# Kernel optimization log

Hardware: AMD Instinct MI355X
Metric: run time of the kernel (lower is better)

Reference implementation:

```python
import jax, jax.numpy as jnp
import numpy as np

DIM = 2048
NUM_HEADS = 16
HEAD_DIM = DIM // NUM_HEADS  # 128
ROPE_BASE = 10000.0


def setup_inputs() -> dict:
    key = jax.random.key(0)
    k1, k2, k3 = jax.random.split(key, 3)
    B, S = 2, 2048
    x = jax.random.normal(k1, (B, S, DIM), dtype=jnp.float32)
    # causal mask: 1 where allowed (k <= q), 0 elsewhere
    mask = jnp.tril(jnp.ones((S, S), dtype=jnp.int32))
    # torch Linear(dim, 3*dim, bias=False): store transposed so y = x @ w
    w_qkv = jax.random.normal(k2, (DIM, 3 * DIM), dtype=jnp.float32) / np.sqrt(DIM)
    w_out = jax.random.normal(k3, (DIM, DIM), dtype=jnp.float32) / np.sqrt(DIM)
    return {"x": x, "w_qkv": w_qkv, "w_out": w_out, "mask": mask}


def _rope_cos_sin(seq_len, dtype):
    inv_freq = 1.0 / (ROPE_BASE ** (jnp.arange(0, HEAD_DIM, 2, dtype=jnp.float32) / HEAD_DIM))
    t = jnp.arange(seq_len, dtype=jnp.float32)
    freqs = t[:, None] * inv_freq[None, :]          # [S, D/2]
    emb = jnp.concatenate([freqs, freqs], axis=-1)  # [S, D]
    return jnp.cos(emb).astype(dtype), jnp.sin(emb).astype(dtype)


def _rotate_half(x):
    x1, x2 = jnp.split(x, 2, axis=-1)
    return jnp.concatenate([-x2, x1], axis=-1)


def reference(x, w_qkv, w_out, mask):
    B, S, _ = x.shape
    H, D = NUM_HEADS, HEAD_DIM
    qkv = x @ w_qkv                                   # [B, S, 3*dim]
    qkv = qkv.reshape(B, S, 3, H, D).transpose(2, 0, 3, 1, 4)  # [3, B, H, S, D]
    q, k, v = qkv[0], qkv[1], qkv[2]
    cos, sin = _rope_cos_sin(S, x.dtype)              # [S, D] broadcast over B,H
    q = q * cos + _rotate_half(q) * sin
    k = k * cos + _rotate_half(k) * sin
    scale = D ** -0.5
    score = jnp.einsum("bhqd,bhkd->bhqk", q, k) * scale
    score = jnp.where(mask == 0, -jnp.inf, score)
    attn = jax.nn.softmax(score, axis=-1)             # dropout = identity (eval)
    out = jnp.einsum("bhqk,bhkd->bhqd", attn, v)
    out = out.transpose(0, 2, 1, 3).reshape(B, S, H * D)
    return out @ w_out
```

## Files before the change

kernel.cpp:

```cpp
#include <hip/hip_runtime.h>

typedef __attribute__((ext_vector_type(8))) __bf16 bf16x8;
typedef __attribute__((ext_vector_type(4))) float f32x4;

__device__ __forceinline__ unsigned short f2bf(float x) {
  union { float f; unsigned int u; } v; v.f = x;
  unsigned int r = v.u + 0x7fffu + ((v.u >> 16) & 1u);
  return (unsigned short)(r >> 16);
}
__device__ __forceinline__ float bf2f(unsigned short x) {
  union { unsigned int u; float f; } v; v.u = ((unsigned int)x) << 16;
  return v.f;
}
__device__ __forceinline__ void g2l16(const void* g, void* l) {
  __builtin_amdgcn_global_load_lds((const __attribute__((address_space(1))) void*)g,
                                   (__attribute__((address_space(3))) void*)l, 16, 0, 0);
}

__global__ __launch_bounds__(256) void cvt_f32_bf16_k(const float* __restrict__ in,
                                                      unsigned short* __restrict__ out) {
  int i = blockIdx.x * 256 + threadIdx.x;
  float4 v = ((const float4*)in)[i];
  ushort4 o;
  o.x = f2bf(v.x); o.y = f2bf(v.y); o.z = f2bf(v.z); o.w = f2bf(v.w);
  ((ushort4*)out)[i] = o;
}

__global__ __launch_bounds__(256) void tr_cvt_k(const float* __restrict__ in,
                                                unsigned short* __restrict__ out,
                                                int R, int C) {
  __shared__ unsigned short t[64][65];
  int c0 = blockIdx.x * 64, r0 = blockIdx.y * 64;
  int tx = threadIdx.x & 63, tg = threadIdx.x >> 6;
#pragma unroll
  for (int i = 0; i < 16; i++) {
    int r = i * 4 + tg;
    t[r][tx] = f2bf(in[(size_t)(r0 + r) * C + c0 + tx]);
  }
  __syncthreads();
#pragma unroll
  for (int i = 0; i < 16; i++) {
    int c = i * 4 + tg;
    out[(size_t)(c0 + c) * R + r0 + tx] = t[tx][c];
  }
}

__global__ __launch_bounds__(256) void tr_b16_k(const unsigned short* __restrict__ in,
                                                unsigned short* __restrict__ out,
                                                int R, int C) {
  __shared__ unsigned short t[64][65];
  const size_t zoff = (size_t)blockIdx.z * R * C;
  int c0 = blockIdx.x * 64, r0 = blockIdx.y * 64;
  int tx = threadIdx.x & 63, tg = threadIdx.x >> 6;
#pragma unroll
  for (int i = 0; i < 16; i++) {
    int r = i * 4 + tg;
    t[r][tx] = in[zoff + (size_t)(r0 + r) * C + c0 + tx];
  }
  __syncthreads();
#pragma unroll
  for (int i = 0; i < 16; i++) {
    int c = i * 4 + tg;
    out[zoff + (size_t)(c0 + c) * R + r0 + tx] = t[tx][c];
  }
}

template <int EPI>
__global__ __launch_bounds__(256) void gemm_bt_k(const unsigned short* __restrict__ A,
                                                 const unsigned short* __restrict__ BT,
                                                 int K, int N,
                                                 float* __restrict__ outF,
                                                 unsigned short* __restrict__ oq,
                                                 unsigned short* __restrict__ ok,
                                                 unsigned short* __restrict__ ov) {
  __shared__ __align__(16) unsigned short lA[128 * 32];
  __shared__ __align__(16) unsigned short lB[128 * 32];
  const int tid = threadIdx.x;
  const int w = tid >> 6, lane = tid & 63;
  const int quad = lane >> 4, l16 = lane & 15;
  const int m0 = blockIdx.y * 128, n0 = blockIdx.x * 128;
  const int wm = (w >> 1) * 64, wn = (w & 1) * 64;
  f32x4 acc[4][4] = {};
  const unsigned short* gA = A + (size_t)(m0 + w * 16 + (lane >> 2)) * K + (lane & 3) * 8;
  const unsigned short* gB = BT + (size_t)(n0 + w * 16 + (lane >> 2)) * K + (lane & 3) * 8;
  char* lAw = (char*)lA + w * 1024 + lane * 16;
  char* lBw = (char*)lB + w * 1024 + lane * 16;
  const size_t rowskip = (size_t)64 * K;
  for (int k0 = 0; k0 < K; k0 += 32) {
    g2l16(gA + k0, lAw);
    g2l16(gA + k0 + rowskip, lAw + 4096);
    g2l16(gB + k0, lBw);
    g2l16(gB + k0 + rowskip, lBw + 4096);
    __syncthreads();
    bf16x8 af[4], bfv[4];
#pragma unroll
    for (int i = 0; i < 4; i++)
      af[i] = *(const bf16x8*)((const char*)lA + (wm + i * 16 + l16) * 64 + quad * 16);
#pragma unroll
    for (int j = 0; j < 4; j++)
      bfv[j] = *(const bf16x8*)((const char*)lB + (wn + j * 16 + l16) * 64 + quad * 16);
#pragma unroll
    for (int i = 0; i < 4; i++)
#pragma unroll
      for (int j = 0; j < 4; j++)
        acc[i][j] = __builtin_amdgcn_mfma_f32_16x16x32_bf16(af[i], bfv[j], acc[i][j], 0, 0, 0);
    __syncthreads();
  }
  if (EPI == 0) {
    const int which = n0 >> 11;
    const int h = (n0 >> 7) & 15;
    unsigned short* dst = (which == 0) ? oq : (which == 1) ? ok : ov;
#pragma unroll
    for (int i = 0; i < 4; i++) {
#pragma unroll
      for (int r = 0; r < 4; r++) {
        int mm = m0 + wm + i * 16 + quad * 4 + r;
        int b = mm >> 11, s = mm & 2047;
        size_t rb = ((size_t)(b * 16 + h) * 2048 + s) * 128;
#pragma unroll
        for (int j = 0; j < 4; j++)
          dst[rb + wn + j * 16 + l16] = f2bf(acc[i][j][r]);
      }
    }
  } else {
#pragma unroll
    for (int i = 0; i < 4; i++)
#pragma unroll
      for (int r = 0; r < 4; r++) {
        size_t rowb = (size_t)(m0 + wm + i * 16 + quad * 4 + r) * N;
#pragma unroll
        for (int j = 0; j < 4; j++)
          outF[rowb + n0 + wn + j * 16 + l16] = acc[i][j][r];
      }
  }
}

__global__ __launch_bounds__(256) void rope_k(unsigned short* __restrict__ buf, float scale) {
  int i = blockIdx.x * 256 + threadIdx.x;
  int d = i & 63;
  int s = (i >> 6) & 2047;
  int bh = i >> 17;
  size_t base = ((size_t)bh * 2048 + s) * 128;
  float a = bf2f(buf[base + d]);
  float b = bf2f(buf[base + 64 + d]);
  double theta = (double)s * exp2(-(double)d * (13.287712379549449 / 64.0));
  double sn, cs;
  sincos(theta, &sn, &cs);
  float c = (float)cs, sf = (float)sn;
  buf[base + d] = f2bf((a * c - b * sf) * scale);
  buf[base + 64 + d] = f2bf((b * c + a * sf) * scale);
}

__global__ __launch_bounds__(256, 2) void attn_k(const unsigned short* __restrict__ qb,
                                                 const unsigned short* __restrict__ kb,
                                                 const unsigned short* __restrict__ vt,
                                                 unsigned short* __restrict__ ob) {
  __shared__ __align__(16) unsigned short lK[64 * 128];
  __shared__ __align__(16) unsigned short lV[128 * 64];
  __shared__ __align__(16) __bf16 pbuf[4][32 * 72];
  const int tid = threadIdx.x;
  const int w = tid >> 6, lane = tid & 63;
  const int quad = lane >> 4, l16 = lane & 15;
  const int qt = (blockIdx.y < 16) ? (int)blockIdx.x : 15 - (int)blockIdx.x;
  const int bh = blockIdx.y;
  const int bi = bh >> 4, h = bh & 15;
  const int q0w = qt * 128 + w * 32;
  const unsigned short* qp = qb + (size_t)bh * 2048 * 128;
  const unsigned short* kp = kb + (size_t)bh * 2048 * 128;
  const unsigned short* vp = vt + (size_t)bh * 128 * 2048;
  __bf16* pw = pbuf[w];

  bf16x8 qf[2][4];
#pragma unroll
  for (int rg = 0; rg < 2; rg++) {
    const unsigned short* qr = qp + (size_t)(q0w + rg * 16 + l16) * 128 + quad * 8;
#pragma unroll
    for (int st = 0; st < 4; st++) qf[rg][st] = *(const bf16x8*)(qr + st * 32);
  }
  f32x4 o[2][8] = {};
  f32x4 lsum[2] = {};

  const int krow = tid >> 4;
  const int kcg = (tid & 15) ^ krow;
  const int vd = tid >> 3;
  const int vsg = (tid & 7) ^ ((tid >> 3) & 7);
  unsigned short* lKdst = lK + (size_t)tid * 8;
  unsigned short* lVdst = lV + (size_t)tid * 8;

  const int nkt = 2 * qt + 2;
  const int myNkt = (q0w + 31) / 64 + 1;
  for (int kt = 0; kt < nkt; kt++) {
    const int kt0 = kt * 64;
#pragma unroll
    for (int j = 0; j < 4; j++) {
      g2l16(kp + (size_t)(kt0 + j * 16 + krow) * 128 + kcg * 8, lKdst + j * 2048);
      g2l16(vp + (size_t)(j * 32 + vd) * 2048 + kt0 + vsg * 8, lVdst + j * 2048);
    }
    __syncthreads();
    if (kt < myNkt) {
      f32x4 sc[2][4] = {};
#pragma unroll
      for (int ct = 0; ct < 4; ct++) {
        const int nrow = ct * 16 + l16;
#pragma unroll
        for (int st = 0; st < 4; st++) {
          bf16x8 kf = *(const bf16x8*)(lK + ((size_t)nrow * 16 + ((st * 4 + quad) ^ l16)) * 8);
          sc[0][ct] = __builtin_amdgcn_mfma_f32_16x16x32_bf16(qf[0][st], kf, sc[0][ct], 0, 0, 0);
          sc[1][ct] = __builtin_amdgcn_mfma_f32_16x16x32_bf16(qf[1][st], kf, sc[1][ct], 0, 0, 0);
        }
      }
      const bool needmask = (kt == myNkt - 1);
#pragma unroll
      for (int rg = 0; rg < 2; rg++)
#pragma unroll
        for (int ct = 0; ct < 4; ct++) {
          const int col = kt0 + ct * 16 + l16;
          const int rowb = q0w + rg * 16 + quad * 4;
#pragma unroll
          for (int r = 0; r < 4; r++) {
            float s = sc[rg][ct][r];
            if (needmask && col > rowb + r) s = -1e30f;
            float e = __expf(s);
            lsum[rg][r] += e;
            pw[(rg * 16 + quad * 4 + r) * 72 + ct * 16 + l16] = (__bf16)e;
          }
        }
      bf16x8 pf[2][2];
#pragma unroll
      for (int rg = 0; rg < 2; rg++)
#pragma unroll
        for (int sb = 0; sb < 2; sb++)
          pf[rg][sb] = *(const bf16x8*)(pw + (rg * 16 + l16) * 72 + sb * 32 + quad * 8);
#pragma unroll
      for (int dt = 0; dt < 8; dt++) {
#pragma unroll
        for (int sb = 0; sb < 2; sb++) {
          bf16x8 vf = *(const bf16x8*)(lV +
              ((size_t)(dt * 16 + l16) * 8 + ((sb * 4 + quad) ^ (l16 & 7))) * 8);
          o[0][dt] = __builtin_amdgcn_mfma_f32_16x16x32_bf16(pf[0][sb], vf, o[0][dt], 0, 0, 0);
          o[1][dt] = __builtin_amdgcn_mfma_f32_16x16x32_bf16(pf[1][sb], vf, o[1][dt], 0, 0, 0);
        }
      }
    }
    __syncthreads();
  }
#pragma unroll
  for (int m = 1; m < 16; m <<= 1)
#pragma unroll
    for (int rg = 0; rg < 2; rg++)
#pragma unroll
      for (int r = 0; r < 4; r++)
        lsum[rg][r] += __shfl_xor(lsum[rg][r], m, 64);
  float inv[2][4];
#pragma unroll
  for (int rg = 0; rg < 2; rg++)
#pragma unroll
    for (int r = 0; r < 4; r++) inv[rg][r] = 1.0f / lsum[rg][r];
#pragma unroll
  for (int rg = 0; rg < 2; rg++)
#pragma unroll
    for (int dt = 0; dt < 8; dt++)
#pragma unroll
      for (int r = 0; r < 4; r++)
        ob[(size_t)(bi * 2048 + q0w + rg * 16 + quad * 4 + r) * 2048 + h * 128 + dt * 16 + l16] =
            f2bf(o[rg][dt][r] * inv[rg][r]);
}

extern "C" void kernel_launch(void* const* d_in, const int* in_sizes, int n_in,
                              void* d_out, int out_size, void* d_ws, size_t ws_size,
                              hipStream_t stream) {
  const float* x = (const float*)d_in[0];
  const float* wqkv = (const float*)d_in[1];
  const float* wout = (const float*)d_in[2];
  char* ws = (char*)d_ws;
  const size_t MiB = 1ull << 20;
  unsigned short* xb    = (unsigned short*)(ws + 0);
  unsigned short* wqkvT = (unsigned short*)(ws + 16 * MiB);
  unsigned short* woutT = (unsigned short*)(ws + 40 * MiB);
  unsigned short* qb    = (unsigned short*)(ws + 48 * MiB);
  unsigned short* kb    = (unsigned short*)(ws + 64 * MiB);
  unsigned short* vb    = (unsigned short*)(ws + 80 * MiB);
  unsigned short* vtb   = (unsigned short*)(ws + 96 * MiB);
  unsigned short* attnb = (unsigned short*)(ws + 112 * MiB);
  float* outF = (float*)d_out;

  cvt_f32_bf16_k<<<8192, 256, 0, stream>>>(x, xb);
  tr_cvt_k<<<dim3(96, 32), 256, 0, stream>>>(wqkv, wqkvT, 2048, 6144);
  tr_cvt_k<<<dim3(32, 32), 256, 0, stream>>>(wout, woutT, 2048, 2048);
  gemm_bt_k<0><<<dim3(48, 32), 256, 0, stream>>>(xb, wqkvT, 2048, 6144, nullptr, qb, kb, vb);
  rope_k<<<16384, 256, 0, stream>>>(qb, 0.08838834764831845f);
  rope_k<<<16384, 256, 0, stream>>>(kb, 1.0f);
  tr_b16_k<<<dim3(2, 32, 32), 256, 0, stream>>>(vb, vtb, 2048, 128);
  attn_k<<<dim3(16, 32), 256, 0, stream>>>(qb, kb, vtb, attnb);
  gemm_bt_k<1><<<dim3(16, 32), 256, 0, stream>>>(attnb, woutT, 2048, 2048, outF,
                                                 nullptr, nullptr, nullptr);
}
```

Before: 447.0 us.

## Widen GEMM K-tile with XOR-swizzled LDS, merge RoPE launches, use fast float trig

The GEMM now stages 64-wide K slices per iteration with an XOR swizzle on LDS chunk placement, which halves the barriers per K and is meant to avoid LDS bank conflicts on fragment reads. The two RoPE launches are merged into one grid that picks q or k from the block index. RoPE angle computation moves from double-precision exp2/sincos to float exp2f and __sincosf. The fast intrinsic loses accuracy for large angles (positions up to 2047), which may hurt numerical agreement with the reference.

```diff
diff --git a/kernel.cpp b/kernel.cpp
--- a/kernel.cpp
+++ b/kernel.cpp
@@ -73,37 +73,45 @@
                                                  unsigned short* __restrict__ oq,
                                                  unsigned short* __restrict__ ok,
                                                  unsigned short* __restrict__ ov) {
-  __shared__ __align__(16) unsigned short lA[128 * 32];
-  __shared__ __align__(16) unsigned short lB[128 * 32];
+  __shared__ __align__(16) unsigned short lA[128 * 64];
+  __shared__ __align__(16) unsigned short lB[128 * 64];
   const int tid = threadIdx.x;
   const int w = tid >> 6, lane = tid & 63;
   const int quad = lane >> 4, l16 = lane & 15;
   const int m0 = blockIdx.y * 128, n0 = blockIdx.x * 128;
   const int wm = (w >> 1) * 64, wn = (w & 1) * 64;
   f32x4 acc[4][4] = {};
-  const unsigned short* gA = A + (size_t)(m0 + w * 16 + (lane >> 2)) * K + (lane & 3) * 8;
-  const unsigned short* gB = BT + (size_t)(n0 + w * 16 + (lane >> 2)) * K + (lane & 3) * 8;
-  char* lAw = (char*)lA + w * 1024 + lane * 16;
-  char* lBw = (char*)lB + w * 1024 + lane * 16;
-  const size_t rowskip = (size_t)64 * K;
-  for (int k0 = 0; k0 < K; k0 += 32) {
-    g2l16(gA + k0, lAw);
-    g2l16(gA + k0 + rowskip, lAw + 4096);
-    g2l16(gB + k0, lBw);
-    g2l16(gB + k0 + rowskip, lBw + 4096);
+  const int srow = tid >> 3;
+  const int schunk = (tid & 7) ^ (srow & 7);
+  const unsigned short* gA = A + (size_t)(m0 + srow) * K + schunk * 8;
+  const unsigned short* gB = BT + (size_t)(n0 + srow) * K + schunk * 8;
+  char* ldA = (char*)lA + tid * 16;
+  char* ldB = (char*)lB + tid * 16;
+  const size_t rskip = (size_t)32 * K;
+  for (int k0 = 0; k0 < K; k0 += 64) {
+#pragma unroll
+    for (int j = 0; j < 4; j++) {
+      g2l16(gA + k0 + j * rskip, ldA + j * 4096);
+      g2l16(gB + k0 + j * rskip, ldB + j * 4096);
+    }
     __syncthreads();
-    bf16x8 af[4], bfv[4];
-#pragma unroll
-    for (int i = 0; i < 4; i++)
-      af[i] = *(const bf16x8*)((const char*)lA + (wm + i * 16 + l16) * 64 + quad * 16);
-#pragma unroll
-    for (int j = 0; j < 4; j++)
-      bfv[j] = *(const bf16x8*)((const char*)lB + (wn + j * 16 + l16) * 64 + quad * 16);
-#pragma unroll
-    for (int i = 0; i < 4; i++)
+#pragma unroll
+    for (int ks = 0; ks < 2; ks++) {
+      bf16x8 af[4], bfv[4];
+#pragma unroll
+      for (int i = 0; i < 4; i++)
+        af[i] = *(const bf16x8*)((const char*)lA + (size_t)(wm + i * 16 + l16) * 128 +
+                                 ((size_t)((ks * 4 + quad) ^ (l16 & 7)) * 16));
 #pragma unroll
       for (int j = 0; j < 4; j++)
-        acc[i][j] = __builtin_amdgcn_mfma_f32_16x16x32_bf16(af[i], bfv[j], acc[i][j], 0, 0, 0);
+        bfv[j] = *(const bf16x8*)((const char*)lB + (size_t)(wn + j * 16 + l16) * 128 +
+                                  ((size_t)((ks * 4 + quad) ^ (l16 & 7)) * 16));
+#pragma unroll
+      for (int i = 0; i < 4; i++)
+#pragma unroll
+        for (int j = 0; j < 4; j++)
+          acc[i][j] = __builtin_amdgcn_mfma_f32_16x16x32_bf16(af[i], bfv[j], acc[i][j], 0, 0, 0);
+    }
     __syncthreads();
   }
   if (EPI == 0) {
@@ -135,20 +143,23 @@
   }
 }
 
-__global__ __launch_bounds__(256) void rope_k(unsigned short* __restrict__ buf, float scale) {
-  int i = blockIdx.x * 256 + threadIdx.x;
+__global__ __launch_bounds__(256) void rope_k(unsigned short* __restrict__ q,
+                                              unsigned short* __restrict__ k) {
+  const int bid = blockIdx.x;
+  unsigned short* buf = (bid < 16384) ? q : k;
+  const float scale = (bid < 16384) ? 0.08838834764831845f : 1.0f;
+  int i = (bid & 16383) * 256 + threadIdx.x;
   int d = i & 63;
   int s = (i >> 6) & 2047;
   int bh = i >> 17;
   size_t base = ((size_t)bh * 2048 + s) * 128;
   float a = bf2f(buf[base + d]);
   float b = bf2f(buf[base + 64 + d]);
-  double theta = (double)s * exp2(-(double)d * (13.287712379549449 / 64.0));
-  double sn, cs;
-  sincos(theta, &sn, &cs);
-  float c = (float)cs, sf = (float)sn;
-  buf[base + d] = f2bf((a * c - b * sf) * scale);
-  buf[base + 64 + d] = f2bf((b * c + a * sf) * scale);
+  float theta = (float)s * exp2f(-(float)d * (13.287712379549449f / 64.0f));
+  float sn, cs;
+  __sincosf(theta, &sn, &cs);
+  buf[base + d] = f2bf((a * cs - b * sn) * scale);
+  buf[base + 64 + d] = f2bf((b * cs + a * sn) * scale);
 }
 
 __global__ __launch_bounds__(256, 2) void attn_k(const unsigned short* __restrict__ qb,
@@ -288,8 +299,7 @@
   tr_cvt_k<<<dim3(96, 32), 256, 0, stream>>>(wqkv, wqkvT, 2048, 6144);
   tr_cvt_k<<<dim3(32, 32), 256, 0, stream>>>(wout, woutT, 2048, 2048);
   gemm_bt_k<0><<<dim3(48, 32), 256, 0, stream>>>(xb, wqkvT, 2048, 6144, nullptr, qb, kb, vb);
-  rope_k<<<16384, 256, 0, stream>>>(qb, 0.08838834764831845f);
-  rope_k<<<16384, 256, 0, stream>>>(kb, 1.0f);
+  rope_k<<<32768, 256, 0, stream>>>(qb, kb);
   tr_b16_k<<<dim3(2, 32, 32), 256, 0, stream>>>(vb, vtb, 2048, 128);
   attn_k<<<dim3(16, 32), 256, 0, stream>>>(qb, kb, vtb, attnb);
   gemm_bt_k<1><<<dim3(16, 32), 256, 0, stream>>>(attnb, woutT, 2048, 2048, outF,
```

Measured after the change: 400.5 us. 10.4% less time.
